# Kernel tuning notes

Measured on AMD Instinct MI355X. Metric: run time of the kernel, lower is better.

The kernel has to match this reference:

```python
import jax, jax.numpy as jnp
import numpy as np

DA_ALPHA = 0.1
DA_LAMDA = 0.5
MAT_DIFF_SCALE = 0.001
KERNEL_MUL = 2.0
KERNEL_NUM = 5

B = 4096
D = 1024
N_CLASSES = 40
K_DIM = 64  # trans_feat is [B, 64, 64]


def setup_inputs() -> dict:
    key = jax.random.key(0)
    k1, k2, k3, k4, k5 = jax.random.split(key, 5)
    logits = jax.random.normal(k1, (B, N_CLASSES), dtype=jnp.float32)
    pred = jax.nn.log_softmax(logits, axis=-1)  # NLL expects log-probs
    target = jax.random.randint(k2, (B,), 0, N_CLASSES, dtype=jnp.int64)
    trans_feat = jax.random.normal(k3, (B, K_DIM, K_DIM), dtype=jnp.float32)
    feature_dense = jax.random.normal(k4, (B, D), dtype=jnp.float32)
    feature_sparse = jax.random.normal(k5, (B, D), dtype=jnp.float32)
    return {
        "pred": pred,
        "target": target,
        "trans_feat": trans_feat,
        "feature_dense": feature_dense,
        "feature_sparse": feature_sparse,
    }


def _nll_loss(pred, target):
    # F.nll_loss with mean reduction: -mean(pred[i, target[i]])
    return -jnp.mean(jnp.take_along_axis(pred, target[:, None], axis=1))


def _feature_transform_regularizer(trans):
    # PointNet: mean over batch of ||I - T T^T||_F
    k = trans.shape[-1]
    eye = jnp.eye(k, dtype=trans.dtype)
    diff = eye - jnp.einsum("bij,bkj->bik", trans, trans)
    return jnp.mean(jnp.sqrt(jnp.sum(diff * diff, axis=(1, 2))))


def _gaussian_kernel_sum(source, target):
    n_samples = source.shape[0] + target.shape[0]
    total = jnp.concatenate([source, target], axis=0)  # [N, D]
    sq = jnp.sum(total * total, axis=-1)  # [N]
    # pairwise squared L2 via GEMM instead of N x N x D broadcast
    l2 = sq[:, None] + sq[None, :] - 2.0 * (total @ total.T)
    l2 = jnp.maximum(l2, 0.0)  # numerical floor (math is >= 0)
    # bandwidth computed from detached distances (torch uses .data)
    bandwidth = jax.lax.stop_gradient(jnp.sum(l2)) / (n_samples ** 2 - n_samples)
    bandwidth = bandwidth / (KERNEL_MUL ** (KERNEL_NUM // 2))
    kernel = jnp.zeros_like(l2)
    for i in range(KERNEL_NUM):
        kernel = kernel + jnp.exp(-l2 / (bandwidth * (KERNEL_MUL ** i)))
    return kernel


def reference(pred, target, trans_feat, feature_dense, feature_sparse):
    loss = _nll_loss(pred, target)
    mat_diff_loss = _feature_transform_regularizer(trans_feat)
    bsz = pred.shape[0]
    kernels = _gaussian_kernel_sum(feature_dense, feature_sparse)  # [2B, 2B]
    xx = jnp.mean(kernels[:bsz, :bsz])
    yy = jnp.mean(kernels[bsz:, bsz:])
    xy = jnp.mean(kernels[:bsz, bsz:])
    yx = jnp.mean(kernels[bsz:, :bsz])
    mmd_loss = xx + yy - xy - yx
    total_loss = DA_ALPHA * loss + mat_diff_loss * MAT_DIFF_SCALE + DA_LAMDA * mmd_loss
    return total_loss
```

## Files before the change

kernel.cpp:

```cpp
#include <hip/hip_runtime.h>
#include <math.h>

#define B_ROWS 4096
#define DIM    1024
#define NTOT   8192
#define NCLS   40
#define TILES2 32
#define NTILE  528
#define NQUAR  64
#define NFULL  512
#define NMATD  512
#define NNLL   8
#define NMAIN  (NQUAR + NFULL + NMATD + NNLL)

typedef __attribute__((ext_vector_type(8))) short bf16x8;
typedef __attribute__((ext_vector_type(4))) float f32x4;

#define WS_TOT_BYTE_OFF 36896

#define MFMA16(d, x, y) d = __builtin_amdgcn_mfma_f32_16x16x32_bf16(x, y, d, 0, 0, 0)

__device__ __forceinline__ unsigned short f2bf(float f) {
  unsigned int u = __float_as_uint(f);
  u += 0x7fffu + ((u >> 16) & 1u);
  return (unsigned short)(u >> 16);
}

__device__ __forceinline__ void async16(const void* g, void* l) {
  __builtin_amdgcn_global_load_lds(
      (const __attribute__((address_space(1))) unsigned int*)g,
      (__attribute__((address_space(3))) unsigned int*)l, 16, 0, 0);
}

__device__ __forceinline__ float wave_sum(float v) {
  v += __shfl_xor(v, 32);
  v += __shfl_xor(v, 16);
  v += __shfl_xor(v, 8);
  v += __shfl_xor(v, 4);
  v += __shfl_xor(v, 2);
  v += __shfl_xor(v, 1);
  return v;
}

__device__ __forceinline__ void decode_tile(int p, int& bi_o, int& bj_o) {
  int bi = (int)((2 * TILES2 + 1 -
                  sqrtf((float)((2 * TILES2 + 1) * (2 * TILES2 + 1) - 8 * p))) * 0.5f);
  if (bi < 0) bi = 0;
  if (bi >= TILES2) bi = TILES2 - 1;
  int start = bi * (2 * TILES2 - bi + 1) / 2;
  while (p < start) { --bi; start = bi * (2 * TILES2 - bi + 1) / 2; }
  while (p >= start + (TILES2 - bi)) { start += TILES2 - bi; ++bi; }
  bi_o = bi; bj_o = bi + (p - start);
}

__global__ __launch_bounds__(256) void prep_k(const float* __restrict__ dense,
                                              const float* __restrict__ sparse,
                                              float* __restrict__ W,
                                              unsigned short* __restrict__ tot) {
  float* colsum = W + 8;
  float* sq = W + 1032;
  const int t = threadIdx.x;
  const int lane = t & 63, wave = t >> 6;
  const int blk = blockIdx.x;
  __shared__ float colsum_l[1024];
  __shared__ float red[4];
  #pragma unroll
  for (int x = 0; x < 4; ++x) colsum_l[t * 4 + x] = 0.f;

  float c[4][4];
  #pragma unroll
  for (int j = 0; j < 4; ++j)
    #pragma unroll
    for (int x = 0; x < 4; ++x) c[j][x] = 0.f;

  float rowtot = 0.f;
  const int rbase = blk * 32 + wave;
  for (int i = 0; i < 8; ++i) {
    const int r = rbase + i * 4;
    const float* src = (r < B_ROWS) ? dense + (size_t)r * DIM
                                    : sparse + (size_t)(r - B_ROWS) * DIM;
    float sp = 0.f;
    #pragma unroll
    for (int j = 0; j < 4; ++j) {
      float4 v = ((const float4*)src)[lane + 64 * j];
      c[j][0] += v.x; c[j][1] += v.y; c[j][2] += v.z; c[j][3] += v.w;
      sp += v.x * v.x + v.y * v.y + v.z * v.z + v.w * v.w;
      ushort4 o;
      o.x = f2bf(v.x); o.y = f2bf(v.y); o.z = f2bf(v.z); o.w = f2bf(v.w);
      *(ushort4*)(tot + (size_t)r * DIM + (lane + 64 * j) * 4) = o;
    }
    sp = wave_sum(sp);
    if (lane == 0) { sq[r] = sp; rowtot += sp; }
  }
  if (lane == 0) red[wave] = rowtot;

  __syncthreads();
  #pragma unroll
  for (int j = 0; j < 4; ++j)
    #pragma unroll
    for (int x = 0; x < 4; ++x)
      atomicAdd(&colsum_l[4 * lane + 256 * j + x], c[j][x]);
  __syncthreads();
  #pragma unroll
  for (int x = 0; x < 4; ++x) {
    const int g = (t * 4 + x + blk * 64) & 1023;
    atomicAdd(&colsum[g], colsum_l[g]);
  }
  if (t == 0) atomicAdd(&W[2], red[0] + red[1] + red[2] + red[3]);
}


struct SmemMain {
  short A[4][8192];
  short B[4][8192];
  float sqA[256], sqB[256], red[8];
};

__device__ void gram_full_body(int p, const unsigned short* __restrict__ tot,
                               float* __restrict__ W, SmemMain& sm) {
  const float* sq = W + 1032;
  const float* colsum = W + 8;
  const int t = threadIdx.x;
  const int lane = t & 63, wave = t >> 6;
  const int wr = wave >> 2, wc = wave & 3;

  int bi, bj;
  decode_tile(p, bi, bj);

  const int r0 = t >> 2;
  const int sg = (t & 3) ^ ((r0 >> 1) & 3);
  const unsigned short* gA0 = tot + (size_t)(bi * 256 + r0) * DIM + sg * 8;
  const unsigned short* gA1 = gA0 + (size_t)128 * DIM;
  const unsigned short* gB0 = tot + (size_t)(bj * 256 + r0) * DIM + sg * 8;
  const unsigned short* gB1 = gB0 + (size_t)128 * DIM;
  const int ldo0 = t * 8, ldo1 = t * 8 + 4096;

  auto stageA = [&](int kt, short* sl) {
    const size_t ko = (size_t)kt * 32;
    async16(gA0 + ko, sl + ldo0);
    async16(gA1 + ko, sl + ldo1);
  };
  auto stageB = [&](int kt, short* sl) {
    const size_t ko = (size_t)kt * 32;
    async16(gB0 + ko, sl + ldo0);
    async16(gB1 + ko, sl + ldo1);
  };

  stageA(0, &sm.A[0][0]); stageB(0, &sm.B[0][0]);
  stageA(1, &sm.A[1][0]); stageB(1, &sm.B[1][0]);
  stageA(2, &sm.A[2][0]); stageB(2, &sm.B[2][0]);

  if (t < 256) sm.sqA[t] = sq[bi * 256 + t];
  else         sm.sqB[t - 256] = sq[bj * 256 + (t - 256)];
  float csp = 0.f;
  #pragma unroll
  for (int j = 0; j < 16; ++j) { float v = colsum[lane + 64 * j]; csp += v * v; }
  csp = wave_sum(csp);
  double sumdots = (double)csp;
  double sum_sq = (double)W[2];
  double sumL2 = 2.0 * (double)NTOT * sum_sq - 2.0 * sumdots;
  double bwv = sumL2 / ((double)NTOT * (double)NTOT - (double)NTOT);
  const float cexp16 = (float)(4.0 / bwv) * 0.0625f;

  f32x4 acc[8][4];
  #pragma unroll
  for (int m = 0; m < 8; ++m)
    #pragma unroll
    for (int n = 0; n < 4; ++n) acc[m][n] = (f32x4)(0.f);

  const int q = lane >> 4;
  const int fr = lane & 15;
  const int rb = (q ^ ((fr >> 1) & 3)) << 4;
  const int aoff = (wr * 128 + fr) * 64 + rb;
  const int boff = (wc * 64 + fr) * 64 + rb;

  asm volatile("s_waitcnt vmcnt(8)" ::: "memory");
  __builtin_amdgcn_s_barrier();

  for (int u = 0; u < 8; ++u) {
    #pragma unroll
    for (int j = 0; j < 4; ++j) {
      const int kt = u * 4 + j;
      const char* cA = (const char*)&sm.A[j][0];
      const char* cB = (const char*)&sm.B[j][0];
      short* stA = &sm.A[(j + 3) & 3][0];
      short* stB = &sm.B[(j + 3) & 3][0];
      const bool st = (kt < 29);

      bf16x8 a[4], b[4];

      #pragma unroll
      for (int m = 0; m < 4; ++m) a[m] = *(const bf16x8*)(cA + aoff + m * 1024);
      #pragma unroll
      for (int n = 0; n < 4; ++n) b[n] = *(const bf16x8*)(cB + boff + n * 1024);
      if (st) stageA(kt + 3, stA);
      __builtin_amdgcn_s_barrier();
      asm volatile("s_waitcnt lgkmcnt(0)" ::: "memory");
      __builtin_amdgcn_s_setprio(1);
      #pragma unroll
      for (int m = 0; m < 4; ++m)
        #pragma unroll
        for (int n = 0; n < 4; ++n) MFMA16(acc[m][n], a[m], b[n]);
      __builtin_amdgcn_s_setprio(0);
      __builtin_amdgcn_s_barrier();

      #pragma unroll
      for (int m = 0; m < 4; ++m) a[m] = *(const bf16x8*)(cA + aoff + (4 + m) * 1024);
      if (st) stageB(kt + 3, stB);
      __builtin_amdgcn_s_barrier();
      asm volatile("s_waitcnt lgkmcnt(0)" ::: "memory");
      __builtin_amdgcn_s_setprio(1);
      #pragma unroll
      for (int m = 0; m < 4; ++m)
        #pragma unroll
        for (int n = 0; n < 4; ++n) MFMA16(acc[4 + m][n], a[m], b[n]);
      __builtin_amdgcn_s_setprio(0);
      if (kt < 29)       { asm volatile("s_waitcnt vmcnt(8)" ::: "memory"); }
      else if (kt == 29) { asm volatile("s_waitcnt vmcnt(4)" ::: "memory"); }
      else if (kt == 30) { asm volatile("s_waitcnt vmcnt(0)" ::: "memory"); }
      __builtin_amdgcn_s_barrier();
    }
  }

  float s = 0.f;
  const int crow = (lane >> 4) * 4;
  #pragma unroll
  for (int m = 0; m < 8; ++m) {
    #pragma unroll
    for (int n = 0; n < 4; ++n) {
      #pragma unroll
      for (int r = 0; r < 4; ++r) {
        int il = wr * 128 + 16 * m + crow + r;
        int jl = wc * 64 + 16 * n + fr;
        float l2 = sm.sqA[il] + sm.sqB[jl] - 2.f * acc[m][n][r];
        l2 = fmaxf(l2, 0.f);
        float k4 = __expf(-l2 * cexp16);
        float k3 = k4 * k4;
        float k2 = k3 * k3;
        float k1 = k2 * k2;
        float k0 = k1 * k1;
        s += k0 + k1 + k2 + k3 + k4;
      }
    }
  }
  s = wave_sum(s);
  if (lane == 0) sm.red[wave] = s;
  __syncthreads();
  if (t == 0) {
    float ts = 0.f;
    #pragma unroll
    for (int w = 0; w < 8; ++w) ts += sm.red[w];
    int idx; float wgt;
    if (bi == bj)      { idx = (bi < 16) ? 3 : 4; wgt = 1.f; }
    else if (bj < 16)  { idx = 3; wgt = 2.f; }
    else if (bi >= 16) { idx = 4; wgt = 2.f; }
    else               { idx = 5; wgt = 2.f; }
    atomicAdd(&W[idx], wgt * ts);
  }
}

__device__ void gram_quarter_body(int p, int quad,
                                  const unsigned short* __restrict__ tot,
                                  float* __restrict__ W, SmemMain& sm) {
  const float* sq = W + 1032;
  const float* colsum = W + 8;
  const int t = threadIdx.x;
  const int lane = t & 63, wave = t >> 6;
  const int wr = wave >> 2, wc = wave & 3;

  int bi, bj;
  decode_tile(p, bi, bj);
  const int h = quad >> 1, v = quad & 1;
  const int rA = bi * 256 + h * 128;
  const int rB = bj * 256 + v * 128;

  const int r0 = t >> 2;
  const int sg = (t & 3) ^ ((r0 >> 1) & 3);
  const unsigned short* gA0 = tot + (size_t)(rA + r0) * DIM + sg * 8;
  const unsigned short* gB0 = tot + (size_t)(rB + r0) * DIM + sg * 8;
  const int ldo = t * 8;

  auto stage = [&](int kt, short* sa, short* sb) {
    const size_t ko = (size_t)kt * 32;
    async16(gA0 + ko, sa + ldo);
    async16(gB0 + ko, sb + ldo);
  };

  stage(0, &sm.A[0][0], &sm.B[0][0]);
  stage(1, &sm.A[1][0], &sm.B[1][0]);
  stage(2, &sm.A[2][0], &sm.B[2][0]);

  if (t < 128)      sm.sqA[t] = sq[rA + t];
  else if (t < 256) sm.sqB[t - 128] = sq[rB + (t - 128)];
  float csp = 0.f;
  #pragma unroll
  for (int j = 0; j < 16; ++j) { float v2 = colsum[lane + 64 * j]; csp += v2 * v2; }
  csp = wave_sum(csp);
  double sumdots = (double)csp;
  double sum_sq = (double)W[2];
  double sumL2 = 2.0 * (double)NTOT * sum_sq - 2.0 * sumdots;
  double bwv = sumL2 / ((double)NTOT * (double)NTOT - (double)NTOT);
  const float cexp16 = (float)(4.0 / bwv) * 0.0625f;

  f32x4 acc[4][2];
  #pragma unroll
  for (int m = 0; m < 4; ++m)
    #pragma unroll
    for (int n = 0; n < 2; ++n) acc[m][n] = (f32x4)(0.f);

  const int q = lane >> 4;
  const int fr = lane & 15;
  const int rb = (q ^ ((fr >> 1) & 3)) << 4;
  const int aoff = (wr * 64 + fr) * 64 + rb;
  const int boff = (wc * 32 + fr) * 64 + rb;

  asm volatile("s_waitcnt vmcnt(4)" ::: "memory");
  __builtin_amdgcn_s_barrier();

  for (int u = 0; u < 8; ++u) {
    #pragma unroll
    for (int j = 0; j < 4; ++j) {
      const int kt = u * 4 + j;
      const char* cA = (const char*)&sm.A[j][0];
      const char* cB = (const char*)&sm.B[j][0];
      short* stA = &sm.A[(j + 3) & 3][0];
      short* stB = &sm.B[(j + 3) & 3][0];

      bf16x8 a[4], b[2];
      #pragma unroll
      for (int m = 0; m < 4; ++m) a[m] = *(const bf16x8*)(cA + aoff + m * 1024);
      #pragma unroll
      for (int n = 0; n < 2; ++n) b[n] = *(const bf16x8*)(cB + boff + n * 1024);
      if (kt < 29) stage(kt + 3, stA, stB);
      __builtin_amdgcn_s_barrier();
      asm volatile("s_waitcnt lgkmcnt(0)" ::: "memory");
      __builtin_amdgcn_s_setprio(1);
      #pragma unroll
      for (int m = 0; m < 4; ++m)
        #pragma unroll
        for (int n = 0; n < 2; ++n) MFMA16(acc[m][n], a[m], b[n]);
      __builtin_amdgcn_s_setprio(0);
      if (kt < 29)       { asm volatile("s_waitcnt vmcnt(4)" ::: "memory"); }
      else if (kt == 29) { asm volatile("s_waitcnt vmcnt(2)" ::: "memory"); }
      else if (kt == 30) { asm volatile("s_waitcnt vmcnt(0)" ::: "memory"); }
      __builtin_amdgcn_s_barrier();
    }
  }

  float s = 0.f;
  const int crow = (lane >> 4) * 4;
  #pragma unroll
  for (int m = 0; m < 4; ++m) {
    #pragma unroll
    for (int n = 0; n < 2; ++n) {
      #pragma unroll
      for (int r = 0; r < 4; ++r) {
        int il = wr * 64 + 16 * m + crow + r;
        int jl = wc * 32 + 16 * n + fr;
        float l2 = sm.sqA[il] + sm.sqB[jl] - 2.f * acc[m][n][r];
        l2 = fmaxf(l2, 0.f);
        float k4 = __expf(-l2 * cexp16);
        float k3 = k4 * k4;
        float k2 = k3 * k3;
        float k1 = k2 * k2;
        float k0 = k1 * k1;
        s += k0 + k1 + k2 + k3 + k4;
      }
    }
  }
  s = wave_sum(s);
  if (lane == 0) sm.red[wave] = s;
  __syncthreads();
  if (t == 0) {
    float ts = 0.f;
    #pragma unroll
    for (int w = 0; w < 8; ++w) ts += sm.red[w];
    int idx; float wgt;
    if (bi == bj)      { idx = (bi < 16) ? 3 : 4; wgt = 1.f; }
    else if (bj < 16)  { idx = 3; wgt = 2.f; }
    else if (bi >= 16) { idx = 4; wgt = 2.f; }
    else               { idx = 5; wgt = 2.f; }
    atomicAdd(&W[idx], wgt * ts);
  }
}

__device__ void nll_body(int bid, const float* __restrict__ pred,
                         const int* __restrict__ tgt, float* __restrict__ W,
                         SmemMain& sm) {
  const int t = threadIdx.x;
  const int i = bid * 512 + t;
  float v = pred[(size_t)i * NCLS + tgt[i]];
  v = wave_sum(v);
  if ((t & 63) == 0) sm.red[t >> 6] = v;
  __syncthreads();
  if (t == 0) {
    float s = 0.f;
    #pragma unroll
    for (int w = 0; w < 8; ++w) s += sm.red[w];
    atomicAdd(&W[0], s);
  }
}

__device__ void matdiff_body(int bid, const float* __restrict__ trans,
                             float* __restrict__ W, SmemMain& sm) {
  const int t = threadIdx.x;
  const int lane = t & 63, wave = t >> 6;
  const int b = bid * 8 + wave;
  const float* Tb = trans + (size_t)b * 4096;
  const int fr = lane & 15;
  const int k8 = (lane >> 4) * 8;
  bf16x8 frag[4][2];
  #pragma unroll
  for (int m = 0; m < 4; ++m) {
    #pragma unroll
    for (int kk = 0; kk < 2; ++kk) {
      const float* p = Tb + (size_t)(16 * m + fr) * 64 + kk * 32 + k8;
      float4 u0 = *(const float4*)p;
      float4 u1 = *(const float4*)(p + 4);
      bf16x8 f;
      f[0] = (short)f2bf(u0.x); f[1] = (short)f2bf(u0.y);
      f[2] = (short)f2bf(u0.z); f[3] = (short)f2bf(u0.w);
      f[4] = (short)f2bf(u1.x); f[5] = (short)f2bf(u1.y);
      f[6] = (short)f2bf(u1.z); f[7] = (short)f2bf(u1.w);
      frag[m][kk] = f;
    }
  }
  f32x4 acc[4][4];
  #pragma unroll
  for (int m = 0; m < 4; ++m)
    #pragma unroll
    for (int n = 0; n < 4; ++n) acc[m][n] = (f32x4)(0.f);
  #pragma unroll
  for (int kk = 0; kk < 2; ++kk)
    #pragma unroll
    for (int m = 0; m < 4; ++m)
      #pragma unroll
      for (int n = 0; n < 4; ++n)
        acc[m][n] = __builtin_amdgcn_mfma_f32_16x16x32_bf16(frag[m][kk], frag[n][kk],
                                                            acc[m][n], 0, 0, 0);
  float s = 0.f;
  const int crow = (lane >> 4) * 4;
  #pragma unroll
  for (int m = 0; m < 4; ++m)
    #pragma unroll
    for (int n = 0; n < 4; ++n)
      #pragma unroll
      for (int r = 0; r < 4; ++r) {
        int grow = 16 * m + crow + r;
        int gcol = 16 * n + fr;
        float g = acc[m][n][r];
        float d = (grow == gcol) ? (1.f - g) : (-g);
        s += d * d;
      }
  s = wave_sum(s);
  if (lane == 0) sm.red[wave] = sqrtf(s);
  __syncthreads();
  if (t == 0) {
    float s8 = 0.f;
    #pragma unroll
    for (int w = 0; w < 8; ++w) s8 += sm.red[w];
    atomicAdd(&W[1], s8);
  }
}

__global__ __launch_bounds__(512, 2) void main_k(
    const float* __restrict__ pred, const int* __restrict__ tgt,
    const float* __restrict__ trans, const unsigned short* __restrict__ tot,
    float* __restrict__ W, float* __restrict__ out) {
  __shared__ SmemMain sm;
  const int blk = blockIdx.x;
  if (blk < NQUAR) {
    gram_quarter_body(512 + (blk >> 2), blk & 3, tot, W, sm);
  } else if (blk < NQUAR + NFULL) {
    const int bfull = blk - NQUAR;
    gram_full_body((bfull & 7) * 64 + (bfull >> 3), tot, W, sm);
  } else if (blk < NQUAR + NFULL + NMATD) {
    matdiff_body(blk - NQUAR - NFULL, trans, W, sm);
  } else {
    nll_body(blk - NQUAR - NFULL - NMATD, pred, tgt, W, sm);
  }

  if (threadIdx.x == 0) {
    __threadfence();
    unsigned int tk = atomicAdd((unsigned int*)(W + 7), 1u);
    if (tk == NMAIN - 1) {
      __threadfence();
      float nll = -*(volatile float*)(W + 0) / (float)B_ROWS;
      float mat =  *(volatile float*)(W + 1) / (float)B_ROWS;
      float sxx =  *(volatile float*)(W + 3);
      float syy =  *(volatile float*)(W + 4);
      float smx =  *(volatile float*)(W + 5);
      float mmd = (sxx + syy - smx) / ((float)B_ROWS * (float)B_ROWS);
      out[0] = 0.1f * nll + 0.001f * mat + 0.5f * mmd;
    }
  }
}

extern "C" void kernel_launch(void* const* d_in, const int* in_sizes, int n_in,
                              void* d_out, int out_size, void* d_ws, size_t ws_size,
                              hipStream_t stream) {
  const float* pred   = (const float*)d_in[0];
  const int*   tgt    = (const int*)d_in[1];
  const float* trans  = (const float*)d_in[2];
  const float* dense  = (const float*)d_in[3];
  const float* sparse = (const float*)d_in[4];
  float* W = (float*)d_ws;
  unsigned short* tot = (unsigned short*)((char*)d_ws + WS_TOT_BYTE_OFF);
  float* out = (float*)d_out;

  hipMemsetAsync(W, 0, 1032 * sizeof(float), stream);
  prep_k<<<dim3(256), dim3(256), 0, stream>>>(dense, sparse, W, tot);
  main_k<<<dim3(NMAIN), dim3(512), 0, stream>>>(pred, tgt, trans, tot, W, out);
}
```

Measured before the change: 168.6 us.

## Split-K the last gram tiles with atomic accumulation and widen prep blocks

New measurement: 186.7 us. 1.11x slower.

```diff
diff --git a/kernel.cpp b/kernel.cpp
--- a/kernel.cpp
+++ b/kernel.cpp
@@ -7,16 +7,18 @@
 #define NCLS   40
 #define TILES2 32
 #define NTILE  528
-#define NQUAR  64
+#define NSPL   64
 #define NFULL  512
 #define NMATD  512
 #define NNLL   8
-#define NMAIN  (NQUAR + NFULL + NMATD + NNLL)
+#define NMAIN  (NSPL + NFULL + NMATD + NNLL)
 
 typedef __attribute__((ext_vector_type(8))) short bf16x8;
 typedef __attribute__((ext_vector_type(4))) float f32x4;
 
 #define WS_TOT_BYTE_OFF 36896
+#define WS_Z_BYTE_OFF   16814112u
+#define WS_NEED_SPLIT   (WS_Z_BYTE_OFF + 4194304u + 64u)
 
 #define MFMA16(d, x, y) d = __builtin_amdgcn_mfma_f32_16x16x32_bf16(x, y, d, 0, 0, 0)
 
@@ -53,7 +55,7 @@
   bi_o = bi; bj_o = bi + (p - start);
 }
 
-__global__ __launch_bounds__(256) void prep_k(const float* __restrict__ dense,
+__global__ __launch_bounds__(512) void prep_k(const float* __restrict__ dense,
                                               const float* __restrict__ sparse,
                                               float* __restrict__ W,
                                               unsigned short* __restrict__ tot) {
@@ -63,9 +65,9 @@
   const int lane = t & 63, wave = t >> 6;
   const int blk = blockIdx.x;
   __shared__ float colsum_l[1024];
-  __shared__ float red[4];
-  #pragma unroll
-  for (int x = 0; x < 4; ++x) colsum_l[t * 4 + x] = 0.f;
+  __shared__ float red[8];
+  colsum_l[t * 2] = 0.f;
+  colsum_l[t * 2 + 1] = 0.f;
 
   float c[4][4];
   #pragma unroll
@@ -74,9 +76,9 @@
     for (int x = 0; x < 4; ++x) c[j][x] = 0.f;
 
   float rowtot = 0.f;
-  const int rbase = blk * 32 + wave;
-  for (int i = 0; i < 8; ++i) {
-    const int r = rbase + i * 4;
+  const int rbase = blk * 32 + wave * 4;
+  for (int i = 0; i < 4; ++i) {
+    const int r = rbase + i;
     const float* src = (r < B_ROWS) ? dense + (size_t)r * DIM
                                     : sparse + (size_t)(r - B_ROWS) * DIM;
     float sp = 0.f;
@@ -102,11 +104,16 @@
       atomicAdd(&colsum_l[4 * lane + 256 * j + x], c[j][x]);
   __syncthreads();
   #pragma unroll
-  for (int x = 0; x < 4; ++x) {
-    const int g = (t * 4 + x + blk * 64) & 1023;
+  for (int x = 0; x < 2; ++x) {
+    const int g = (t * 2 + x + blk * 64) & 1023;
     atomicAdd(&colsum[g], colsum_l[g]);
   }
-  if (t == 0) atomicAdd(&W[2], red[0] + red[1] + red[2] + red[3]);
+  if (t == 0) {
+    float s = 0.f;
+    #pragma unroll
+    for (int w = 0; w < 8; ++w) s += red[w];
+    atomicAdd(&W[2], s);
+  }
 }
 
 
@@ -114,24 +121,27 @@
   short A[4][8192];
   short B[4][8192];
   float sqA[256], sqB[256], red[8];
+  int itick;
 };
 
-__device__ void gram_full_body(int p, const unsigned short* __restrict__ tot,
-                               float* __restrict__ W, SmemMain& sm) {
+template<int NKT, bool PART>
+__device__ void gram_body_t(int bi, int bj, int k0,
+                            const unsigned short* __restrict__ tot,
+                            float* __restrict__ W,
+                            float* __restrict__ Z,
+                            unsigned int* __restrict__ ztick,
+                            SmemMain& sm) {
   const float* sq = W + 1032;
   const float* colsum = W + 8;
   const int t = threadIdx.x;
   const int lane = t & 63, wave = t >> 6;
   const int wr = wave >> 2, wc = wave & 3;
 
-  int bi, bj;
-  decode_tile(p, bi, bj);
-
   const int r0 = t >> 2;
   const int sg = (t & 3) ^ ((r0 >> 1) & 3);
-  const unsigned short* gA0 = tot + (size_t)(bi * 256 + r0) * DIM + sg * 8;
+  const unsigned short* gA0 = tot + (size_t)(bi * 256 + r0) * DIM + sg * 8 + (size_t)k0 * 32;
   const unsigned short* gA1 = gA0 + (size_t)128 * DIM;
-  const unsigned short* gB0 = tot + (size_t)(bj * 256 + r0) * DIM + sg * 8;
+  const unsigned short* gB0 = tot + (size_t)(bj * 256 + r0) * DIM + sg * 8 + (size_t)k0 * 32;
   const unsigned short* gB1 = gB0 + (size_t)128 * DIM;
   const int ldo0 = t * 8, ldo1 = t * 8 + 4096;
 
@@ -177,7 +187,7 @@
   asm volatile("s_waitcnt vmcnt(8)" ::: "memory");
   __builtin_amdgcn_s_barrier();
 
-  for (int u = 0; u < 8; ++u) {
+  for (int u = 0; u < NKT / 4; ++u) {
     #pragma unroll
     for (int j = 0; j < 4; ++j) {
       const int kt = u * 4 + j;
@@ -185,7 +195,7 @@
       const char* cB = (const char*)&sm.B[j][0];
       short* stA = &sm.A[(j + 3) & 3][0];
       short* stB = &sm.B[(j + 3) & 3][0];
-      const bool st = (kt < 29);
+      const bool st = (kt < NKT - 3);
 
       bf16x8 a[4], b[4];
 
@@ -215,47 +225,93 @@
         #pragma unroll
         for (int n = 0; n < 4; ++n) MFMA16(acc[4 + m][n], a[m], b[n]);
       __builtin_amdgcn_s_setprio(0);
-      if (kt < 29)       { asm volatile("s_waitcnt vmcnt(8)" ::: "memory"); }
-      else if (kt == 29) { asm volatile("s_waitcnt vmcnt(4)" ::: "memory"); }
-      else if (kt == 30) { asm volatile("s_waitcnt vmcnt(0)" ::: "memory"); }
+      if (kt < NKT - 3)       { asm volatile("s_waitcnt vmcnt(8)" ::: "memory"); }
+      else if (kt == NKT - 3) { asm volatile("s_waitcnt vmcnt(4)" ::: "memory"); }
+      else if (kt == NKT - 2) { asm volatile("s_waitcnt vmcnt(0)" ::: "memory"); }
       __builtin_amdgcn_s_barrier();
     }
   }
 
-  float s = 0.f;
   const int crow = (lane >> 4) * 4;
-  #pragma unroll
-  for (int m = 0; m < 8; ++m) {
-    #pragma unroll
-    for (int n = 0; n < 4; ++n) {
-      #pragma unroll
-      for (int r = 0; r < 4; ++r) {
-        int il = wr * 128 + 16 * m + crow + r;
-        int jl = wc * 64 + 16 * n + fr;
-        float l2 = sm.sqA[il] + sm.sqB[jl] - 2.f * acc[m][n][r];
-        l2 = fmaxf(l2, 0.f);
+
+  if (!PART) {
+    float s = 0.f;
+    #pragma unroll
+    for (int m = 0; m < 8; ++m) {
+      #pragma unroll
+      for (int n = 0; n < 4; ++n) {
+        #pragma unroll
+        for (int r = 0; r < 4; ++r) {
+          int il = wr * 128 + 16 * m + crow + r;
+          int jl = wc * 64 + 16 * n + fr;
+          float l2 = sm.sqA[il] + sm.sqB[jl] - 2.f * acc[m][n][r];
+          l2 = fmaxf(l2, 0.f);
+          float k4 = __expf(-l2 * cexp16);
+          float k3 = k4 * k4;
+          float k2 = k3 * k3;
+          float k1 = k2 * k2;
+          float k0f = k1 * k1;
+          s += k0f + k1 + k2 + k3 + k4;
+        }
+      }
+    }
+    s = wave_sum(s);
+    if (lane == 0) sm.red[wave] = s;
+    __syncthreads();
+    if (t == 0) {
+      float ts = 0.f;
+      #pragma unroll
+      for (int w = 0; w < 8; ++w) ts += sm.red[w];
+      int idx; float wgt;
+      if (bi == bj)      { idx = (bi < 16) ? 3 : 4; wgt = 1.f; }
+      else if (bj < 16)  { idx = 3; wgt = 2.f; }
+      else if (bi >= 16) { idx = 4; wgt = 2.f; }
+      else               { idx = 5; wgt = 2.f; }
+      atomicAdd(&W[idx], wgt * ts);
+    }
+  } else {
+    #pragma unroll
+    for (int m = 0; m < 8; ++m)
+      #pragma unroll
+      for (int n = 0; n < 4; ++n)
+        #pragma unroll
+        for (int r = 0; r < 4; ++r) {
+          int il = wr * 128 + 16 * m + crow + r;
+          int jl = wc * 64 + 16 * n + fr;
+          atomicAdd(&Z[il * 256 + jl], acc[m][n][r]);
+        }
+    __threadfence();
+    if (t == 0) sm.itick = (int)atomicAdd(ztick, 1u);
+    __syncthreads();
+    if (sm.itick == 3) {
+      float s = 0.f;
+      for (int idx = t; idx < 65536; idx += 512) {
+        float z = __hip_atomic_load(Z + idx, __ATOMIC_RELAXED,
+                                    __HIP_MEMORY_SCOPE_AGENT);
+        int il = idx >> 8, jl = idx & 255;
+        float l2 = fmaxf(sm.sqA[il] + sm.sqB[jl] - 2.f * z, 0.f);
         float k4 = __expf(-l2 * cexp16);
         float k3 = k4 * k4;
         float k2 = k3 * k3;
         float k1 = k2 * k2;
-        float k0 = k1 * k1;
-        s += k0 + k1 + k2 + k3 + k4;
+        float k0f = k1 * k1;
+        s += k0f + k1 + k2 + k3 + k4;
       }
-    }
-  }
-  s = wave_sum(s);
-  if (lane == 0) sm.red[wave] = s;
-  __syncthreads();
-  if (t == 0) {
-    float ts = 0.f;
-    #pragma unroll
-    for (int w = 0; w < 8; ++w) ts += sm.red[w];
-    int idx; float wgt;
-    if (bi == bj)      { idx = (bi < 16) ? 3 : 4; wgt = 1.f; }
-    else if (bj < 16)  { idx = 3; wgt = 2.f; }
-    else if (bi >= 16) { idx = 4; wgt = 2.f; }
-    else               { idx = 5; wgt = 2.f; }
-    atomicAdd(&W[idx], wgt * ts);
+      s = wave_sum(s);
+      if (lane == 0) sm.red[wave] = s;
+      __syncthreads();
+      if (t == 0) {
+        float ts = 0.f;
+        #pragma unroll
+        for (int w = 0; w < 8; ++w) ts += sm.red[w];
+        int idx; float wgt;
+        if (bi == bj)      { idx = (bi < 16) ? 3 : 4; wgt = 1.f; }
+        else if (bj < 16)  { idx = 3; wgt = 2.f; }
+        else if (bi >= 16) { idx = 4; wgt = 2.f; }
+        else               { idx = 5; wgt = 2.f; }
+        atomicAdd(&W[idx], wgt * ts);
+      }
+    }
   }
 }
 
@@ -466,18 +522,29 @@
 __global__ __launch_bounds__(512, 2) void main_k(
     const float* __restrict__ pred, const int* __restrict__ tgt,
     const float* __restrict__ trans, const unsigned short* __restrict__ tot,
-    float* __restrict__ W, float* __restrict__ out) {
+    float* __restrict__ W, float* __restrict__ Z,
+    unsigned int* __restrict__ ztick, int use_split,
+    float* __restrict__ out) {
   __shared__ SmemMain sm;
   const int blk = blockIdx.x;
-  if (blk < NQUAR) {
-    gram_quarter_body(512 + (blk >> 2), blk & 3, tot, W, sm);
-  } else if (blk < NQUAR + NFULL) {
-    const int bfull = blk - NQUAR;
-    gram_full_body((bfull & 7) * 64 + (bfull >> 3), tot, W, sm);
-  } else if (blk < NQUAR + NFULL + NMATD) {
-    matdiff_body(blk - NQUAR - NFULL, trans, W, sm);
+  if (blk < NSPL) {
+    const int zi = blk >> 2, kq = blk & 3;
+    int bi, bj;
+    decode_tile(512 + zi, bi, bj);
+    if (use_split) {
+      gram_body_t<8, true>(bi, bj, kq * 8, tot, W, Z + zi * 65536, ztick + zi, sm);
+    } else {
+      gram_quarter_body(512 + zi, kq, tot, W, sm);
+    }
+  } else if (blk < NSPL + NFULL) {
+    const int bfull = blk - NSPL;
+    int bi, bj;
+    decode_tile((bfull & 7) * 64 + (bfull >> 3), bi, bj);
+    gram_body_t<32, false>(bi, bj, 0, tot, W, Z, ztick, sm);
+  } else if (blk < NSPL + NFULL + NMATD) {
+    matdiff_body(blk - NSPL - NFULL, trans, W, sm);
   } else {
-    nll_body(blk - NQUAR - NFULL - NMATD, pred, tgt, W, sm);
+    nll_body(blk - NSPL - NFULL - NMATD, pred, tgt, W, sm);
   }
 
   if (threadIdx.x == 0) {
@@ -506,9 +573,16 @@
   const float* sparse = (const float*)d_in[4];
   float* W = (float*)d_ws;
   unsigned short* tot = (unsigned short*)((char*)d_ws + WS_TOT_BYTE_OFF);
+  float* Z = (float*)((char*)d_ws + WS_Z_BYTE_OFF);
+  unsigned int* ztick = (unsigned int*)((char*)d_ws + WS_Z_BYTE_OFF + 4194304u);
   float* out = (float*)d_out;
 
+  const int use_split = (ws_size >= (size_t)WS_NEED_SPLIT) ? 1 : 0;
+
   hipMemsetAsync(W, 0, 1032 * sizeof(float), stream);
-  prep_k<<<dim3(256), dim3(256), 0, stream>>>(dense, sparse, W, tot);
-  main_k<<<dim3(NMAIN), dim3(512), 0, stream>>>(pred, tgt, trans, tot, W, out);
-}
+  if (use_split)
+    hipMemsetAsync((char*)d_ws + WS_Z_BYTE_OFF, 0, 4194304u + 64u, stream);
+  prep_k<<<dim3(256), dim3(512), 0, stream>>>(dense, sparse, W, tot);
+  main_k<<<dim3(NMAIN), dim3(512), 0, stream>>>(pred, tgt, trans, tot, W,
+                                                Z, ztick, use_split, out);
+}
```
